# Kernel optimization log

Hardware: AMD Instinct MI355X
Metric: run time of the kernel (lower is better)

## Reference

```python
import jax, jax.numpy as jnp
import numpy as np

N_NODES = 131072   # rows of node_mars
MAX_ELS = 65600    # rows of element_mars
N_PROD = 65536     # number of product nodes in this partition
N_EDGES = 4        # children per product node
BATCH = 512


def setup_inputs() -> dict:
    key = jax.random.key(0)
    k1, k2 = jax.random.split(key)
    node_mars = jax.random.normal(k1, (N_NODES, BATCH), dtype=jnp.float32)
    element_mars = jnp.zeros((MAX_ELS, BATCH), dtype=jnp.float32)
    nids = jnp.arange(N_PROD, dtype=jnp.int64)  # unique scatter targets
    cids = jax.random.randint(k2, (N_PROD, N_EDGES), 0, N_NODES, dtype=jnp.int64)
    return {"node_mars": node_mars, "element_mars": element_mars,
            "nids": nids, "cids": cids}


def reference(node_mars, element_mars, nids, cids):
    # ProdLayer.forward (block_size == 1, single partition, accum=False):
    #   element_mars[nids] = node_mars[cids].sum(dim=1)
    # Gather child log-marginals and sum over the children axis (product of
    # probabilities == sum of log-probs), then scatter into element_mars.
    vals = node_mars[cids].sum(axis=1)            # [N_PROD, BATCH]
    return element_mars.at[nids].set(vals)        # [MAX_ELS, BATCH]
```

## Files before the change

### kernel.cpp

```cpp
#include <hip/hip_runtime.h>


constexpr int BATCH   = 512;
constexpr int N_PROD  = 65536;
constexpr int MAX_ELS = 65600;
constexpr int N_EDGES = 4;
constexpr int VEC     = 4;
constexpr int LANES   = BATCH / VEC;
constexpr int ROWS_PER_BLOCK = 2;

typedef float f32x4 __attribute__((ext_vector_type(4)));

__global__ __launch_bounds__(256) void ProdLayer_69750268887705_kernel(
    const float* __restrict__ node_mars,
    const float* __restrict__ element_mars,
    const int*   __restrict__ nids,
    const int*   __restrict__ cids,
    float*       __restrict__ out)
{
    const int tid   = threadIdx.x;
    const int rsub  = tid >> 7;
    const int lane  = tid & (LANES - 1);
    const int p     = blockIdx.x * ROWS_PER_BLOCK + rsub;
    if (p >= MAX_ELS) return;

    if (p < N_PROD) {
        const int out_row = nids[p];
        const int c0 = cids[p * N_EDGES + 0];
        const int c1 = cids[p * N_EDGES + 1];
        const int c2 = cids[p * N_EDGES + 2];
        const int c3 = cids[p * N_EDGES + 3];
        const f32x4* r0 = (const f32x4*)(node_mars + (size_t)c0 * BATCH);
        const f32x4* r1 = (const f32x4*)(node_mars + (size_t)c1 * BATCH);
        const f32x4* r2 = (const f32x4*)(node_mars + (size_t)c2 * BATCH);
        const f32x4* r3 = (const f32x4*)(node_mars + (size_t)c3 * BATCH);
        f32x4 a = r0[lane];
        f32x4 b = r1[lane];
        f32x4 c = r2[lane];
        f32x4 d = r3[lane];
        f32x4 s = (a + b) + (c + d);
        __builtin_nontemporal_store(s, (f32x4*)(out + (size_t)out_row * BATCH) + lane);
    } else {
        f32x4 v = ((const f32x4*)(element_mars + (size_t)p * BATCH))[lane];
        __builtin_nontemporal_store(v, (f32x4*)(out + (size_t)p * BATCH) + lane);
    }
}

extern "C" void kernel_launch(void* const* d_in, const int* in_sizes, int n_in,
                              void* d_out, int out_size, void* d_ws, size_t ws_size,
                              hipStream_t stream) {
    const float* node_mars    = (const float*)d_in[0];
    const float* element_mars = (const float*)d_in[1];
    const int*   nids         = (const int*)d_in[2];
    const int*   cids         = (const int*)d_in[3];
    float*       out          = (float*)d_out;

    const int nBlocks = (MAX_ELS + ROWS_PER_BLOCK - 1) / ROWS_PER_BLOCK;
    ProdLayer_69750268887705_kernel<<<nBlocks, 256, 0, stream>>>(
        node_mars, element_mars, nids, cids, out);
}
```

Before: 98.70 us.

## Split batch into column chunks so each block handles more product rows

The kernel now splits the 512-wide batch into four column chunks. Each block covers 8 product rows over one 128-column chunk, and blocks are ordered chunk-major so that one chunk's working set of gathered node_mars columns is smaller and more likely to be reused in L2/MALL. The four child indices are loaded with a single vector load, and nontemporal stores become regular stores. The cost is that each cids/nids entry is read four times, and rows are touched in 512-byte pieces instead of whole 2 KB rows.

```diff
diff --git a/kernel.cpp b/kernel.cpp
--- a/kernel.cpp
+++ b/kernel.cpp
@@ -1,15 +1,18 @@
 #include <hip/hip_runtime.h>
 
 
-constexpr int BATCH   = 512;
-constexpr int N_PROD  = 65536;
-constexpr int MAX_ELS = 65600;
-constexpr int N_EDGES = 4;
-constexpr int VEC     = 4;
-constexpr int LANES   = BATCH / VEC;
-constexpr int ROWS_PER_BLOCK = 2;
+constexpr int BATCH    = 512;
+constexpr int N_PROD   = 65536;
+constexpr int MAX_ELS  = 65600;
+constexpr int N_EDGES  = 4;
+constexpr int CHUNKS   = 4;
+constexpr int CHUNK_W  = BATCH / CHUNKS;
+constexpr int LANES    = CHUNK_W / 4;
+constexpr int PROD_PER_BLOCK = 256 / LANES;
+constexpr int BLOCKS_PER_CHUNK = MAX_ELS / PROD_PER_BLOCK;
 
 typedef float f32x4 __attribute__((ext_vector_type(4)));
+typedef int   i32x4 __attribute__((ext_vector_type(4)));
 
 __global__ __launch_bounds__(256) void ProdLayer_69750268887705_kernel(
     const float* __restrict__ node_mars,
@@ -18,31 +21,28 @@
     const int*   __restrict__ cids,
     float*       __restrict__ out)
 {
-    const int tid   = threadIdx.x;
-    const int rsub  = tid >> 7;
-    const int lane  = tid & (LANES - 1);
-    const int p     = blockIdx.x * ROWS_PER_BLOCK + rsub;
-    if (p >= MAX_ELS) return;
+    const int tid  = threadIdx.x;
+    const int lane = tid & (LANES - 1);
+    const int psub = tid >> 5;
+
+    const int chunk = blockIdx.x / BLOCKS_PER_CHUNK;
+    const int bic   = blockIdx.x - chunk * BLOCKS_PER_CHUNK;
+    const int p     = bic * PROD_PER_BLOCK + psub;
+
+    const int col4 = chunk * (CHUNK_W / 4) + lane;
 
     if (p < N_PROD) {
         const int out_row = nids[p];
-        const int c0 = cids[p * N_EDGES + 0];
-        const int c1 = cids[p * N_EDGES + 1];
-        const int c2 = cids[p * N_EDGES + 2];
-        const int c3 = cids[p * N_EDGES + 3];
-        const f32x4* r0 = (const f32x4*)(node_mars + (size_t)c0 * BATCH);
-        const f32x4* r1 = (const f32x4*)(node_mars + (size_t)c1 * BATCH);
-        const f32x4* r2 = (const f32x4*)(node_mars + (size_t)c2 * BATCH);
-        const f32x4* r3 = (const f32x4*)(node_mars + (size_t)c3 * BATCH);
-        f32x4 a = r0[lane];
-        f32x4 b = r1[lane];
-        f32x4 c = r2[lane];
-        f32x4 d = r3[lane];
-        f32x4 s = (a + b) + (c + d);
-        __builtin_nontemporal_store(s, (f32x4*)(out + (size_t)out_row * BATCH) + lane);
+        const i32x4 c = *(const i32x4*)(cids + (size_t)p * N_EDGES);
+        const f32x4 a = *((const f32x4*)(node_mars + (size_t)c.x * BATCH) + col4);
+        const f32x4 b = *((const f32x4*)(node_mars + (size_t)c.y * BATCH) + col4);
+        const f32x4 d = *((const f32x4*)(node_mars + (size_t)c.z * BATCH) + col4);
+        const f32x4 e = *((const f32x4*)(node_mars + (size_t)c.w * BATCH) + col4);
+        const f32x4 s = (a + b) + (d + e);
+        *((f32x4*)(out + (size_t)out_row * BATCH) + col4) = s;
     } else {
-        f32x4 v = ((const f32x4*)(element_mars + (size_t)p * BATCH))[lane];
-        __builtin_nontemporal_store(v, (f32x4*)(out + (size_t)p * BATCH) + lane);
+        *((f32x4*)(out + (size_t)p * BATCH) + col4) =
+            *((const f32x4*)(element_mars + (size_t)p * BATCH) + col4);
     }
 }
 
@@ -55,7 +55,7 @@
     const int*   cids         = (const int*)d_in[3];
     float*       out          = (float*)d_out;
 
-    const int nBlocks = (MAX_ELS + ROWS_PER_BLOCK - 1) / ROWS_PER_BLOCK;
+    const int nBlocks = CHUNKS * BLOCKS_PER_CHUNK;
     ProdLayer_69750268887705_kernel<<<nBlocks, 256, 0, stream>>>(
         node_mars, element_mars, nids, cids, out);
 }
```

Measured after the change: 95.95 us. 2.8% less time.
